# Performance work log

Measured on AMD Instinct MI355X. Metric: run time of the kernel, lower is better.

## Reference

```python
import jax, jax.numpy as jnp
import numpy as np

I, H, O = 64, 256, 24
B, S = 256, 1024


def setup_inputs() -> dict:
    key = jax.random.key(0)
    ks = jax.random.split(key, 9)
    s = lambda *d: 1.0 / np.sqrt(d[0])
    return {
        "x": jax.random.normal(ks[0], (B, S, I), dtype=jnp.float32),
        "Wi": jax.random.normal(ks[1], (I, 4 * H), dtype=jnp.float32) * s(I),
        "Wh": jax.random.normal(ks[2], (H, 4 * H), dtype=jnp.float32) * s(H),
        "b": jnp.zeros((4 * H,), dtype=jnp.float32),
        "attn_W": jax.random.normal(ks[3], (H, H), dtype=jnp.float32) * s(H),
        "attn_b": jnp.zeros((H,), dtype=jnp.float32),
        "v": jax.random.uniform(ks[4], (H,), dtype=jnp.float32) * 0.01,
        "fc_W": jax.random.normal(ks[5], (H, O), dtype=jnp.float32) * s(H),
        "fc_b": jnp.zeros((O,), dtype=jnp.float32),
    }


def _lstm(x, Wi, Wh, b):
    # x: [B, S, I] -> outputs [B, S, H]
    xW = jnp.einsum("bsi,ij->bsj", x, Wi)  # precompute input projections
    Bsz = x.shape[0]
    h0 = jnp.zeros((Bsz, H), x.dtype)
    c0 = jnp.zeros((Bsz, H), x.dtype)

    def step(carry, xt):
        c, h = carry
        z = xt + h @ Wh + b  # [B, 4H]
        i, f, g, o = jnp.split(z, 4, axis=-1)
        c = jax.nn.sigmoid(f) * c + jax.nn.sigmoid(i) * jnp.tanh(g)
        h = jax.nn.sigmoid(o) * jnp.tanh(c)
        return (c, h), h

    _, hs = jax.lax.scan(step, (c0, h0), jnp.swapaxes(xW, 0, 1))
    return jnp.swapaxes(hs, 0, 1)  # [B, S, H]


def reference(x, Wi, Wh, b, attn_W, attn_b, v, fc_W, fc_b):
    lstm_out = _lstm(x, Wi, Wh, b)  # [B, S, H]
    energy = jnp.tanh(lstm_out @ attn_W + attn_b)  # [B, S, H]
    scores = jnp.einsum("bsh,h->bs", energy, v)
    attn = jax.nn.softmax(scores, axis=1)  # [B, S]
    context = jnp.einsum("bs,bsh->bh", attn, lstm_out)
    return context @ fc_W + fc_b  # [B, O]
```

## Files before the change

### kernel.cpp

```cpp
#include <hip/hip_runtime.h>

#define BB 256
#define SS 1024
#define II 64
#define HH 256
#define OO 24
#define NG 16
#define NP 16
#define BT 16

typedef __attribute__((ext_vector_type(8))) short short8;
typedef __attribute__((ext_vector_type(4))) float f32x4;
typedef unsigned long long ull;

#define H_CAP  8192
#define SP_CAP 16384

#define A_HI 0
#define A_LO 8192
#define Z_OF 16384
#define E_OF 20480
#define SMEM_BYTES 98304

#define MFMA(a,b,c) __builtin_amdgcn_mfma_f32_16x16x32_bf16(a,b,c,0,0,0)

__device__ __forceinline__ float fsig(float x)  { return 1.f/(1.f+__expf(-x)); }
__device__ __forceinline__ float ftanh(float x) { return 1.f - 2.f/(__expf(2.f*x)+1.f); }

__device__ __forceinline__ unsigned rne_bf16(float x){
    unsigned u = __float_as_uint(x);
    return (u + 0x7FFFu + ((u>>16)&1u)) >> 16;
}
__device__ __forceinline__ void split_bf(float x, unsigned &hi, unsigned &lo){
    hi = rne_bf16(x);
    lo = rne_bf16(x - __uint_as_float(hi<<16));
}

union U4 { unsigned u[4]; short8 s; };

__device__ __forceinline__ void pack8(const float* v, short8 &H, short8 &L){
    U4 h_, l_;
    #pragma unroll
    for (int i = 0; i < 4; ++i) {
        unsigned a,b,c,d;
        split_bf(v[2*i], a, b); split_bf(v[2*i+1], c, d);
        h_.u[i] = a | (c<<16);
        l_.u[i] = b | (d<<16);
    }
    H = h_.s; L = l_.s;
}

__device__ __forceinline__ ull cld(const ull* p){
    return __hip_atomic_load(p, __ATOMIC_RELAXED, __HIP_MEMORY_SCOPE_AGENT);
}
__device__ __forceinline__ void cst(ull* p, ull v){
    __hip_atomic_store(p, v, __ATOMIC_RELAXED, __HIP_MEMORY_SCOPE_AGENT);
}

__global__ __launch_bounds__(256, 1)
void lstm_fused_kernel(const float* __restrict__ x,  const float* __restrict__ Wi,
                       const float* __restrict__ Wh, const float* __restrict__ bias,
                       const float* __restrict__ aW, const float* __restrict__ ab,
                       const float* __restrict__ av,
                       ull* __restrict__ hx, ull* __restrict__ spx,
                       float* __restrict__ ctxg)
{
    __shared__ __align__(16) char smem[SMEM_BYTES];
    __shared__ int sdead;

    const int tid = threadIdx.x;
    const int w = tid >> 6;
    const int l = tid & 63;
    const int p = blockIdx.x >> 4;
    const int g = blockIdx.x & 15;
    const int b0 = g * BT;

    if (tid == 0) sdead = 0;
    __syncthreads();

    const int n = l & 15;
    const int gcol = w*256 + p*16 + n;
    const int gb = (l>>4)*4 + w;
    const int gd = n;

    short8 BwhH[8], BwhL[8];
    #pragma unroll
    for (int ks = 0; ks < 8; ++ks) {
        U4 H, L;
        #pragma unroll
        for (int i2 = 0; i2 < 4; ++i2) {
            int k0 = ks*32 + (l>>4)*8 + i2*2;
            unsigned h0,l0,h1,l1;
            split_bf(Wh[(size_t)k0*1024 + gcol], h0, l0);
            split_bf(Wh[(size_t)(k0+1)*1024 + gcol], h1, l1);
            H.u[i2] = h0 | (h1<<16);
            L.u[i2] = l0 | (l1<<16);
        }
        BwhH[ks] = H.s; BwhL[ks] = L.s;
    }
    short8 BwiH[2], BwiL[2];
    #pragma unroll
    for (int ks = 0; ks < 2; ++ks) {
        U4 H, L;
        #pragma unroll
        for (int i2 = 0; i2 < 4; ++i2) {
            int k0 = ks*32 + (l>>4)*8 + i2*2;
            unsigned h0,l0,h1,l1;
            split_bf(Wi[(size_t)k0*1024 + gcol], h0, l0);
            split_bf(Wi[(size_t)(k0+1)*1024 + gcol], h1, l1);
            H.u[i2] = h0 | (h1<<16);
            L.u[i2] = l0 | (l1<<16);
        }
        BwiH[ks] = H.s; BwiL[ks] = L.s;
    }
    short8 BwaH[2], BwaL[2];
    #pragma unroll
    for (int j = 0; j < 2; ++j) {
        int ks = 2*w + j;
        U4 H, L;
        #pragma unroll
        for (int i2 = 0; i2 < 4; ++i2) {
            int k0 = ks*32 + (l>>4)*8 + i2*2;
            unsigned h0,l0,h1,l1;
            split_bf(aW[(size_t)k0*256 + p*16 + n], h0, l0);
            split_bf(aW[(size_t)(k0+1)*256 + p*16 + n], h1, l1);
            H.u[i2] = h0 | (h1<<16);
            L.u[i2] = l0 | (l1<<16);
        }
        BwaH[j] = H.s; BwaL[j] = L.s;
    }
    const float bb  = bias[gcol];
    const float vj  = av[p*16 + gd];
    const float abj = ab[p*16 + gd];

    const int po    = tid >> 3;
    const int pbase = (tid & 7) * 2;
    const int wa0 = (po>>2)*1024 + ((po&3)*16 + pbase)*16;
    const int wa1 = wa0 + 16;

    const int D = p*16 + gd;
    const int tau   = (gb>>1) | ((D>>3)<<3);
    const int j_pub = ((gb&1)<<3) | (D&7);

    const int xb = l & 15;
    const int xoct = l >> 4;

    float c_state = 0.f, h1v = 0.f, h2v = 0.f;
    float m_run = -1.0e30f, l_run = 0.f, ctx = 0.f;

    float* zl = (float*)(smem + Z_OF);
    float* el = (float*)(smem + E_OF);

    for (int t = 0; t < SS; ++t) {
        const int par = t & 1;
        const float* xrow = x + ((size_t)(b0 + xb) * SS + t) * II + xoct*8;
        float xv0[8], xv1[8];
        *(float4*)&xv0[0] = *(const float4*)(xrow);
        *(float4*)&xv0[4] = *(const float4*)(xrow + 4);
        *(float4*)&xv1[0] = *(const float4*)(xrow + 32);
        *(float4*)&xv1[4] = *(const float4*)(xrow + 36);

        ull hv[16]; ull spr = 0;
        const ull* hr = hx + ((size_t)(((t-1)&1)*NG + g) * 16) * 256 + tid;
        if (t > 0) {
            #pragma unroll
            for (int j = 0; j < 16; ++j) hv[j] = cld(hr + j*256);
        }
        ull* spp = spx + (size_t)par*4096 + g*256 + gb*16 + gd;
        if (t > 1) spr = cld(spp);

        short8 XH0, XL0, XH1, XL1;
        pack8(xv0, XH0, XL0);
        pack8(xv1, XH1, XL1);
        f32x4 zacc = {bb,bb,bb,bb};
        zacc = MFMA(XH0, BwiH[0], zacc);
        zacc = MFMA(XH0, BwiL[0], zacc);
        zacc = MFMA(XL0, BwiH[0], zacc);
        zacc = MFMA(XH1, BwiH[1], zacc);
        zacc = MFMA(XH1, BwiL[1], zacc);
        zacc = MFMA(XL1, BwiH[1], zacc);

        if (t > 0) {
            const unsigned texp = (unsigned)t;
            unsigned need = 0xFFFFu;
            int rounds = 0;
            while (true) {
                unsigned nn = 0;
                #pragma unroll
                for (int e = 0; e < 16; ++e)
                    if (need & (1u<<e))
                        if ((unsigned)(hv[e]>>32) != texp) nn |= (1u<<e);
                need = nn;
                if (!need || sdead) break;
                if (++rounds > H_CAP) { sdead = 1; break; }
                #pragma unroll
                for (int e = 0; e < 16; ++e)
                    if (need & (1u<<e)) hv[e] = cld(hr + e*256);
            }
            float va[16];
            #pragma unroll
            for (int e = 0; e < 16; ++e) va[e] = __uint_as_float((unsigned)hv[e]);
            short8 H0,L0,H1,L1;
            pack8(&va[0], H0, L0);
            pack8(&va[8], H1, L1);
            *(short8*)(smem + A_HI + wa0) = H0;
            *(short8*)(smem + A_LO + wa0) = L0;
            *(short8*)(smem + A_HI + wa1) = H1;
            *(short8*)(smem + A_LO + wa1) = L1;
        }
        __syncthreads();

        f32x4 zacc1 = {0.f,0.f,0.f,0.f};
        f32x4 eacc  = {0.f,0.f,0.f,0.f};
        if (t > 0) {
            #pragma unroll
            for (int ks = 0; ks < 8; ++ks) {
                short8 ah = *(const short8*)(smem + A_HI + ks*1024 + l*16);
                short8 al = *(const short8*)(smem + A_LO + ks*1024 + l*16);
                if ((ks & 1) == 0) {
                    zacc = MFMA(ah, BwhH[ks], zacc);
                    zacc = MFMA(ah, BwhL[ks], zacc);
                    zacc = MFMA(al, BwhH[ks], zacc);
                } else {
                    zacc1 = MFMA(ah, BwhH[ks], zacc1);
                    zacc1 = MFMA(ah, BwhL[ks], zacc1);
                    zacc1 = MFMA(al, BwhH[ks], zacc1);
                }
                if ((ks>>1) == w) {
                    int jj = ks & 1;
                    eacc = MFMA(ah, BwaH[jj], eacc);
                    eacc = MFMA(ah, BwaL[jj], eacc);
                    eacc = MFMA(al, BwaH[jj], eacc);
                }
            }
        }
        #pragma unroll
        for (int r = 0; r < 4; ++r) zl[w*256 + r*64 + l] = zacc[r] + zacc1[r];
        if (t > 0) {
            #pragma unroll
            for (int r = 0; r < 4; ++r) el[w*256 + r*64 + l] = eacc[r];
        }
        __syncthreads();

        float z0 = zl[0*256 + w*64 + l];
        float z1 = zl[1*256 + w*64 + l];
        float z2 = zl[2*256 + w*64 + l];
        float z3 = zl[3*256 + w*64 + l];
        float ig = fsig(z0), fg = fsig(z1), gv = ftanh(z2), og = fsig(z3);
        c_state = fg*c_state + ig*gv;
        float h = og * ftanh(c_state);

        cst(hx + ((size_t)(par*NG + g) * 16 + j_pub) * 256 + tau,
            ((ull)(unsigned)(t+1) << 32) | (ull)__float_as_uint(h));

        if (t > 0) {
            float e = el[0*256+w*64+l] + el[1*256+w*64+l]
                    + el[2*256+w*64+l] + el[3*256+w*64+l] + abj;
            float scp = vj * ftanh(e);
            scp += __shfl_xor(scp,1); scp += __shfl_xor(scp,2);
            scp += __shfl_xor(scp,4); scp += __shfl_xor(scp,8);
            if (gd == 0)
                cst(spx + (size_t)((t-1)&1)*4096 + g*256 + gb*16 + p,
                    ((ull)(unsigned)t << 32) | (ull)__float_as_uint(scp));
        }
        if (t > 1) {
            const unsigned texp = (unsigned)(t-1);
            int it = 0;
            while ((unsigned)(spr>>32) != texp) {
                if (sdead || ++it > SP_CAP) { sdead = 1; break; }
                spr = cld(spp);
            }
            float s = __uint_as_float((unsigned)spr);
            s += __shfl_xor(s,1); s += __shfl_xor(s,2);
            s += __shfl_xor(s,4); s += __shfl_xor(s,8);
            float m_new = fmaxf(m_run, s);
            float sc = __expf(m_run - m_new);
            float wt = __expf(s - m_new);
            l_run = l_run*sc + wt;
            ctx   = ctx*sc + wt*h2v;
            m_run = m_new;
        }
        h2v = h1v; h1v = h;
    }

    {
        const ull* hr = hx + ((size_t)(((SS-1)&1)*NG + g) * 16) * 256 + tid;
        ull hv[16];
        #pragma unroll
        for (int j = 0; j < 16; ++j) hv[j] = cld(hr + j*256);
        const unsigned texp = (unsigned)SS;
        unsigned need = 0xFFFFu;
        int rounds = 0;
        while (true) {
            unsigned nn = 0;
            #pragma unroll
            for (int e = 0; e < 16; ++e)
                if (need & (1u<<e))
                    if ((unsigned)(hv[e]>>32) != texp) nn |= (1u<<e);
            need = nn;
            if (!need || sdead) break;
            if (++rounds > H_CAP) { sdead = 1; break; }
            #pragma unroll
            for (int e = 0; e < 16; ++e)
                if (need & (1u<<e)) hv[e] = cld(hr + e*256);
        }
        float va[16];
        #pragma unroll
        for (int e = 0; e < 16; ++e) va[e] = __uint_as_float((unsigned)hv[e]);
        short8 H0,L0,H1,L1;
        pack8(&va[0], H0, L0);
        pack8(&va[8], H1, L1);
        *(short8*)(smem + A_HI + wa0) = H0;
        *(short8*)(smem + A_LO + wa0) = L0;
        *(short8*)(smem + A_HI + wa1) = H1;
        *(short8*)(smem + A_LO + wa1) = L1;
        __syncthreads();

        f32x4 eacc = {0.f,0.f,0.f,0.f};
        #pragma unroll
        for (int ks = 0; ks < 8; ++ks) {
            if ((ks>>1) == w) {
                short8 ah = *(const short8*)(smem + A_HI + ks*1024 + l*16);
                short8 al = *(const short8*)(smem + A_LO + ks*1024 + l*16);
                int jj = ks & 1;
                eacc = MFMA(ah, BwaH[jj], eacc);
                eacc = MFMA(ah, BwaL[jj], eacc);
                eacc = MFMA(al, BwaH[jj], eacc);
            }
        }
        #pragma unroll
        for (int r = 0; r < 4; ++r) el[w*256 + r*64 + l] = eacc[r];
        __syncthreads();

        {
            ull* spp2 = spx + (size_t)(SS&1)*4096 + g*256 + gb*16 + gd;
            ull spr = cld(spp2);
            const unsigned te2 = (unsigned)(SS-1);
            int it = 0;
            while ((unsigned)(spr>>32) != te2) {
                if (sdead || ++it > SP_CAP) { sdead = 1; break; }
                spr = cld(spp2);
            }
            float s = __uint_as_float((unsigned)spr);
            s += __shfl_xor(s,1); s += __shfl_xor(s,2);
            s += __shfl_xor(s,4); s += __shfl_xor(s,8);
            float m_new = fmaxf(m_run, s);
            float sc = __expf(m_run - m_new);
            float wt = __expf(s - m_new);
            l_run = l_run*sc + wt;
            ctx   = ctx*sc + wt*h2v;
            m_run = m_new;
        }
        h2v = h1v;
        float e = el[0*256+w*64+l] + el[1*256+w*64+l]
                + el[2*256+w*64+l] + el[3*256+w*64+l] + abj;
        float scp = vj * ftanh(e);
        scp += __shfl_xor(scp,1); scp += __shfl_xor(scp,2);
        scp += __shfl_xor(scp,4); scp += __shfl_xor(scp,8);
        if (gd == 0)
            cst(spx + (size_t)((SS-1)&1)*4096 + g*256 + gb*16 + p,
                ((ull)(unsigned)SS << 32) | (ull)__float_as_uint(scp));
    }

    {
        ull* spp2 = spx + (size_t)((SS-1)&1)*4096 + g*256 + gb*16 + gd;
        ull spr = cld(spp2);
        const unsigned texp = (unsigned)SS;
        int it = 0;
        while ((unsigned)(spr>>32) != texp) {
            if (sdead || ++it > SP_CAP) { sdead = 1; break; }
            spr = cld(spp2);
        }
        float s = __uint_as_float((unsigned)spr);
        s += __shfl_xor(s,1); s += __shfl_xor(s,2);
        s += __shfl_xor(s,4); s += __shfl_xor(s,8);
        float m_new = fmaxf(m_run, s);
        float sc = __expf(m_run - m_new);
        float wt = __expf(s - m_new);
        l_run = l_run*sc + wt;
        ctx   = ctx*sc + wt*h2v;

        ctxg[(size_t)(b0+gb)*HH + p*16 + gd] = ctx / l_run;
    }
}

__global__ __launch_bounds__(64)
void finalize_kernel(const float* __restrict__ ctxg, const float* __restrict__ fcW,
                     const float* __restrict__ fcb, float* __restrict__ out)
{
    __shared__ float cs[HH];
    const int b = blockIdx.x, tid = threadIdx.x;
    *(float4*)&cs[tid*4] = *(const float4*)&ctxg[(size_t)b*HH + tid*4];
    __syncthreads();
    if (tid < OO) {
        float a = fcb[tid];
        #pragma unroll 8
        for (int d = 0; d < HH; ++d) a = fmaf(cs[d], fcW[d*OO + tid], a);
        out[b*OO + tid] = a;
    }
}

extern "C" void kernel_launch(void* const* d_in, const int* in_sizes, int n_in,
                              void* d_out, int out_size, void* d_ws, size_t ws_size,
                              hipStream_t stream)
{
    const float* x      = (const float*)d_in[0];
    const float* Wi     = (const float*)d_in[1];
    const float* Wh     = (const float*)d_in[2];
    const float* bias   = (const float*)d_in[3];
    const float* attn_W = (const float*)d_in[4];
    const float* attn_b = (const float*)d_in[5];
    const float* v      = (const float*)d_in[6];
    const float* fc_W   = (const float*)d_in[7];
    const float* fc_b   = (const float*)d_in[8];
    float* out = (float*)d_out;

    ull*   hx   = (ull*)d_ws;
    ull*   spx  = hx + 2*NG*16*256;
    float* ctxg = (float*)(spx + 8192);

    hipMemsetAsync(hx, 0, (2*NG*16*256 + 8192) * sizeof(ull), stream);

    lstm_fused_kernel<<<dim3(NG*NP), dim3(256), 0, stream>>>(
        x, Wi, Wh, bias, attn_W, attn_b, v, hx, spx, ctxg);
    finalize_kernel<<<dim3(BB), dim3(64), 0, stream>>>(ctxg, fc_W, fc_b, out);
}
```

Measured before the change: 3.523 ms.

## Permute gate columns so gate exchange uses shuffles and pre-split published h

New measurement: 3.569 ms. Within noise of the previous version (+1.3%).

```diff
diff --git a/kernel.cpp b/kernel.cpp
--- a/kernel.cpp
+++ b/kernel.cpp
@@ -18,8 +18,8 @@
 
 #define A_HI 0
 #define A_LO 8192
-#define Z_OF 16384
-#define E_OF 20480
+#define E_OF 16384
+#define HLOC 20480
 #define SMEM_BYTES 98304
 
 #define MFMA(a,b,c) __builtin_amdgcn_mfma_f32_16x16x32_bf16(a,b,c,0,0,0)
@@ -79,9 +79,18 @@
     __syncthreads();
 
     const int n = l & 15;
-    const int gcol = w*256 + p*16 + n;
-    const int gb = (l>>4)*4 + w;
-    const int gd = n;
+    const int gcol = (n>>2)*256 + p*16 + w*4 + (n&3);
+
+    const int sb  = (l>>4)*4 + w;
+    const int sjd = n;
+
+    const int cch = l >> 3, t3 = l & 7;
+    const int b_g  = (t3<<1) | (cch>>2);
+    const int D_gl = 4*w + (cch&3);
+    const int breg = ((t3&1)<<1) | (cch>>2);
+    const int srcb = ((t3>>1)<<4) | (cch&3);
+    const int j_pub = ((b_g&1)<<3) | (D_gl&7);
+    const int tau   = ((2*p + (D_gl>>3))<<3) | t3;
 
     short8 BwhH[8], BwhL[8];
     #pragma unroll
@@ -130,26 +139,22 @@
         BwaH[j] = H.s; BwaL[j] = L.s;
     }
     const float bb  = bias[gcol];
-    const float vj  = av[p*16 + gd];
-    const float abj = ab[p*16 + gd];
+    const float vj  = av[p*16 + sjd];
+    const float abj = ab[p*16 + sjd];
 
     const int po    = tid >> 3;
     const int pbase = (tid & 7) * 2;
     const int wa0 = (po>>2)*1024 + ((po&3)*16 + pbase)*16;
     const int wa1 = wa0 + 16;
 
-    const int D = p*16 + gd;
-    const int tau   = (gb>>1) | ((D>>3)<<3);
-    const int j_pub = ((gb&1)<<3) | (D&7);
-
     const int xb = l & 15;
     const int xoct = l >> 4;
 
-    float c_state = 0.f, h1v = 0.f, h2v = 0.f;
+    float c_state = 0.f;
     float m_run = -1.0e30f, l_run = 0.f, ctx = 0.f;
 
-    float* zl = (float*)(smem + Z_OF);
-    float* el = (float*)(smem + E_OF);
+    float* el   = (float*)(smem + E_OF);
+    float* hloc = (float*)(smem + HLOC);
 
     for (int t = 0; t < SS; ++t) {
         const int par = t & 1;
@@ -166,7 +171,7 @@
             #pragma unroll
             for (int j = 0; j < 16; ++j) hv[j] = cld(hr + j*256);
         }
-        ull* spp = spx + (size_t)par*4096 + g*256 + gb*16 + gd;
+        ull* spp = spx + (size_t)par*4096 + g*256 + sb*16 + sjd;
         if (t > 1) spr = cld(spp);
 
         short8 XH0, XL0, XH1, XL1;
@@ -197,16 +202,20 @@
                 for (int e = 0; e < 16; ++e)
                     if (need & (1u<<e)) hv[e] = cld(hr + e*256);
             }
-            float va[16];
-            #pragma unroll
-            for (int e = 0; e < 16; ++e) va[e] = __uint_as_float((unsigned)hv[e]);
-            short8 H0,L0,H1,L1;
-            pack8(&va[0], H0, L0);
-            pack8(&va[8], H1, L1);
-            *(short8*)(smem + A_HI + wa0) = H0;
-            *(short8*)(smem + A_LO + wa0) = L0;
-            *(short8*)(smem + A_HI + wa1) = H1;
-            *(short8*)(smem + A_LO + wa1) = L1;
+            U4 H0u, L0u, H1u, L1u;
+            #pragma unroll
+            for (int i = 0; i < 4; ++i) {
+                unsigned a = (unsigned)hv[2*i],   b_ = (unsigned)hv[2*i+1];
+                unsigned c = (unsigned)hv[8+2*i], d_ = (unsigned)hv[9+2*i];
+                H0u.u[i] = (a>>16) | (b_ & 0xFFFF0000u);
+                L0u.u[i] = (a & 0xFFFFu) | (b_<<16);
+                H1u.u[i] = (c>>16) | (d_ & 0xFFFF0000u);
+                L1u.u[i] = (c & 0xFFFFu) | (d_<<16);
+            }
+            *(short8*)(smem + A_HI + wa0) = H0u.s;
+            *(short8*)(smem + A_LO + wa0) = L0u.s;
+            *(short8*)(smem + A_HI + wa1) = H1u.s;
+            *(short8*)(smem + A_LO + wa1) = L1u.s;
         }
         __syncthreads();
 
@@ -234,24 +243,41 @@
                 }
             }
         }
-        #pragma unroll
-        for (int r = 0; r < 4; ++r) zl[w*256 + r*64 + l] = zacc[r] + zacc1[r];
-        if (t > 0) {
-            #pragma unroll
-            for (int r = 0; r < 4; ++r) el[w*256 + r*64 + l] = eacc[r];
-        }
-        __syncthreads();
-
-        float z0 = zl[0*256 + w*64 + l];
-        float z1 = zl[1*256 + w*64 + l];
-        float z2 = zl[2*256 + w*64 + l];
-        float z3 = zl[3*256 + w*64 + l];
-        float ig = fsig(z0), fg = fsig(z1), gv = ftanh(z2), og = fsig(z3);
+
+        float zs0 = zacc[0]+zacc1[0], zs1 = zacc[1]+zacc1[1];
+        float zs2 = zacc[2]+zacc1[2], zs3 = zacc[3]+zacc1[3];
+        float zg0,zg1,zg2,zg3;
+        #pragma unroll
+        for (int q = 0; q < 4; ++q) {
+            int srcl = srcb | (q<<2);
+            float v0 = __shfl(zs0, srcl);
+            float v1 = __shfl(zs1, srcl);
+            float v2 = __shfl(zs2, srcl);
+            float v3 = __shfl(zs3, srcl);
+            float vv = (breg==0)? v0 : (breg==1)? v1 : (breg==2)? v2 : v3;
+            if      (q==0) zg0 = vv;
+            else if (q==1) zg1 = vv;
+            else if (q==2) zg2 = vv;
+            else           zg3 = vv;
+        }
+        float ig = fsig(zg0), fg = fsig(zg1), gv = ftanh(zg2), og = fsig(zg3);
         c_state = fg*c_state + ig*gv;
         float h = og * ftanh(c_state);
 
-        cst(hx + ((size_t)(par*NG + g) * 16 + j_pub) * 256 + tau,
-            ((ull)(unsigned)(t+1) << 32) | (ull)__float_as_uint(h));
+        hloc[((t%3)*16 + b_g)*17 + D_gl] = h;
+
+        {
+            unsigned hhi, hlo;
+            split_bf(h, hhi, hlo);
+            cst(hx + ((size_t)(par*NG + g) * 16 + j_pub) * 256 + tau,
+                ((ull)(unsigned)(t+1) << 32) | (ull)((hhi<<16)|hlo));
+        }
+
+        if (t > 0) {
+            #pragma unroll
+            for (int r = 0; r < 4; ++r) el[w*256 + r*64 + l] = eacc[r];
+        }
+        __syncthreads();
 
         if (t > 0) {
             float e = el[0*256+w*64+l] + el[1*256+w*64+l]
@@ -259,8 +285,8 @@
             float scp = vj * ftanh(e);
             scp += __shfl_xor(scp,1); scp += __shfl_xor(scp,2);
             scp += __shfl_xor(scp,4); scp += __shfl_xor(scp,8);
-            if (gd == 0)
-                cst(spx + (size_t)((t-1)&1)*4096 + g*256 + gb*16 + p,
+            if (sjd == 0)
+                cst(spx + (size_t)((t-1)&1)*4096 + g*256 + sb*16 + p,
                     ((ull)(unsigned)t << 32) | (ull)__float_as_uint(scp));
         }
         if (t > 1) {
@@ -273,14 +299,14 @@
             float s = __uint_as_float((unsigned)spr);
             s += __shfl_xor(s,1); s += __shfl_xor(s,2);
             s += __shfl_xor(s,4); s += __shfl_xor(s,8);
+            float hh = hloc[(((t-2)%3)*16 + sb)*17 + sjd];
             float m_new = fmaxf(m_run, s);
             float sc = __expf(m_run - m_new);
             float wt = __expf(s - m_new);
             l_run = l_run*sc + wt;
-            ctx   = ctx*sc + wt*h2v;
+            ctx   = ctx*sc + wt*hh;
             m_run = m_new;
         }
-        h2v = h1v; h1v = h;
     }
 
     {
@@ -304,16 +330,20 @@
             for (int e = 0; e < 16; ++e)
                 if (need & (1u<<e)) hv[e] = cld(hr + e*256);
         }
-        float va[16];
-        #pragma unroll
-        for (int e = 0; e < 16; ++e) va[e] = __uint_as_float((unsigned)hv[e]);
-        short8 H0,L0,H1,L1;
-        pack8(&va[0], H0, L0);
-        pack8(&va[8], H1, L1);
-        *(short8*)(smem + A_HI + wa0) = H0;
-        *(short8*)(smem + A_LO + wa0) = L0;
-        *(short8*)(smem + A_HI + wa1) = H1;
-        *(short8*)(smem + A_LO + wa1) = L1;
+        U4 H0u, L0u, H1u, L1u;
+        #pragma unroll
+        for (int i = 0; i < 4; ++i) {
+            unsigned a = (unsigned)hv[2*i],   b_ = (unsigned)hv[2*i+1];
+            unsigned c = (unsigned)hv[8+2*i], d_ = (unsigned)hv[9+2*i];
+            H0u.u[i] = (a>>16) | (b_ & 0xFFFF0000u);
+            L0u.u[i] = (a & 0xFFFFu) | (b_<<16);
+            H1u.u[i] = (c>>16) | (d_ & 0xFFFF0000u);
+            L1u.u[i] = (c & 0xFFFFu) | (d_<<16);
+        }
+        *(short8*)(smem + A_HI + wa0) = H0u.s;
+        *(short8*)(smem + A_LO + wa0) = L0u.s;
+        *(short8*)(smem + A_HI + wa1) = H1u.s;
+        *(short8*)(smem + A_LO + wa1) = L1u.s;
         __syncthreads();
 
         f32x4 eacc = {0.f,0.f,0.f,0.f};
@@ -333,7 +363,7 @@
         __syncthreads();
 
         {
-            ull* spp2 = spx + (size_t)(SS&1)*4096 + g*256 + gb*16 + gd;
+            ull* spp2 = spx + (size_t)(SS&1)*4096 + g*256 + sb*16 + sjd;
             ull spr = cld(spp2);
             const unsigned te2 = (unsigned)(SS-1);
             int it = 0;
@@ -344,26 +374,26 @@
             float s = __uint_as_float((unsigned)spr);
             s += __shfl_xor(s,1); s += __shfl_xor(s,2);
             s += __shfl_xor(s,4); s += __shfl_xor(s,8);
+            float hh = hloc[(((SS-2)%3)*16 + sb)*17 + sjd];
             float m_new = fmaxf(m_run, s);
             float sc = __expf(m_run - m_new);
             float wt = __expf(s - m_new);
             l_run = l_run*sc + wt;
-            ctx   = ctx*sc + wt*h2v;
+            ctx   = ctx*sc + wt*hh;
             m_run = m_new;
         }
-        h2v = h1v;
         float e = el[0*256+w*64+l] + el[1*256+w*64+l]
                 + el[2*256+w*64+l] + el[3*256+w*64+l] + abj;
         float scp = vj * ftanh(e);
         scp += __shfl_xor(scp,1); scp += __shfl_xor(scp,2);
         scp += __shfl_xor(scp,4); scp += __shfl_xor(scp,8);
-        if (gd == 0)
-            cst(spx + (size_t)((SS-1)&1)*4096 + g*256 + gb*16 + p,
+        if (sjd == 0)
+            cst(spx + (size_t)((SS-1)&1)*4096 + g*256 + sb*16 + p,
                 ((ull)(unsigned)SS << 32) | (ull)__float_as_uint(scp));
     }
 
     {
-        ull* spp2 = spx + (size_t)((SS-1)&1)*4096 + g*256 + gb*16 + gd;
+        ull* spp2 = spx + (size_t)((SS-1)&1)*4096 + g*256 + sb*16 + sjd;
         ull spr = cld(spp2);
         const unsigned texp = (unsigned)SS;
         int it = 0;
@@ -374,13 +404,14 @@
         float s = __uint_as_float((unsigned)spr);
         s += __shfl_xor(s,1); s += __shfl_xor(s,2);
         s += __shfl_xor(s,4); s += __shfl_xor(s,8);
+        float hh = hloc[(((SS-1)%3)*16 + sb)*17 + sjd];
         float m_new = fmaxf(m_run, s);
         float sc = __expf(m_run - m_new);
         float wt = __expf(s - m_new);
         l_run = l_run*sc + wt;
-        ctx   = ctx*sc + wt*h2v;
-
-        ctxg[(size_t)(b0+gb)*HH + p*16 + gd] = ctx / l_run;
+        ctx   = ctx*sc + wt*hh;
+
+        ctxg[(size_t)(b0+sb)*HH + p*16 + sjd] = ctx / l_run;
     }
 }
 
```

## Interleave two independent batch streams per block to hide cross-block latency

Applied to the files above, without the earlier changes.

Result: slower. 6.389 ms (+81.4%).

```diff
diff --git a/kernel.cpp b/kernel.cpp
--- a/kernel.cpp
+++ b/kernel.cpp
@@ -5,9 +5,9 @@
 #define II 64
 #define HH 256
 #define OO 24
-#define NG 16
+#define NG 32
 #define NP 16
-#define BT 16
+#define BT 8
 
 typedef __attribute__((ext_vector_type(8))) short short8;
 typedef __attribute__((ext_vector_type(4))) float f32x4;
@@ -16,10 +16,14 @@
 #define H_CAP  8192
 #define SP_CAP 16384
 
-#define A_HI 0
-#define A_LO 8192
-#define Z_OF 16384
-#define E_OF 20480
+#define AHI_A 0
+#define ALO_A 8192
+#define AHI_B 16384
+#define ALO_B 24576
+#define ZL_A  32768
+#define EL_A  36864
+#define ZL_B  40960
+#define EL_B  45056
 #define SMEM_BYTES 98304
 
 #define MFMA(a,b,c) __builtin_amdgcn_mfma_f32_16x16x32_bf16(a,b,c,0,0,0)
@@ -57,217 +61,122 @@
     __hip_atomic_store(p, v, __ATOMIC_RELAXED, __HIP_MEMORY_SCOPE_AGENT);
 }
 
-__global__ __launch_bounds__(256, 1)
-void lstm_fused_kernel(const float* __restrict__ x,  const float* __restrict__ Wi,
-                       const float* __restrict__ Wh, const float* __restrict__ bias,
-                       const float* __restrict__ aW, const float* __restrict__ ab,
-                       const float* __restrict__ av,
-                       ull* __restrict__ hx, ull* __restrict__ spx,
-                       float* __restrict__ ctxg)
-{
-    __shared__ __align__(16) char smem[SMEM_BYTES];
-    __shared__ int sdead;
-
-    const int tid = threadIdx.x;
-    const int w = tid >> 6;
-    const int l = tid & 63;
-    const int p = blockIdx.x >> 4;
-    const int g = blockIdx.x & 15;
-    const int b0 = g * BT;
-
-    if (tid == 0) sdead = 0;
-    __syncthreads();
-
-    const int n = l & 15;
-    const int gcol = w*256 + p*16 + n;
-    const int gb = (l>>4)*4 + w;
-    const int gd = n;
-
-    short8 BwhH[8], BwhL[8];
-    #pragma unroll
-    for (int ks = 0; ks < 8; ++ks) {
+template<int AHI, int ALO, int ZLo, int ELo>
+__device__ __forceinline__ void stream_step(
+    int t, int tid, int w, int l, int p, int g, int b0,
+    const float* __restrict__ x, char* smem, int* sdp,
+    const short8* BwhH, const short8* BwhL,
+    const short8* BwiH, const short8* BwiL,
+    const short8* BwaH, const short8* BwaL,
+    float bbv, float vj, float abj,
+    ull* hx, ull* spx, ull* hv,
+    float& c_state, float& h1v, float& h2v,
+    float& m_run, float& l_run, float& ctx)
+{
+    const int xb = l & 7, xoct = l >> 4;
+    const float* xrow = x + ((size_t)(b0 + xb) * SS + t) * II + xoct*8;
+    float xv0[8], xv1[8];
+    *(float4*)&xv0[0] = *(const float4*)(xrow);
+    *(float4*)&xv0[4] = *(const float4*)(xrow + 4);
+    *(float4*)&xv1[0] = *(const float4*)(xrow + 32);
+    *(float4*)&xv1[4] = *(const float4*)(xrow + 36);
+
+    const int sb  = tid >> 4;
+    const int sjd = tid & 15;
+    ull spr = 0;
+    ull* spp = spx + (size_t)((t&1)*NG + g)*128 + (sb&7)*16 + sjd;
+    if (t > 1 && tid < 128) spr = cld(spp);
+
+    short8 XH0,XL0,XH1,XL1;
+    pack8(xv0,XH0,XL0); pack8(xv1,XH1,XL1);
+    f32x4 zacc = {bbv,bbv,bbv,bbv};
+    zacc = MFMA(XH0,BwiH[0],zacc); zacc = MFMA(XH0,BwiL[0],zacc); zacc = MFMA(XL0,BwiH[0],zacc);
+    zacc = MFMA(XH1,BwiH[1],zacc); zacc = MFMA(XH1,BwiL[1],zacc); zacc = MFMA(XL1,BwiH[1],zacc);
+
+    if (t > 0) {
+        const ull* hr = hx + ((size_t)(((t-1)&1)*NG + g)*8)*256 + tid;
+        const unsigned texp = (unsigned)t;
+        unsigned need = 0xFFu; int rounds = 0;
+        while (true) {
+            unsigned nn = 0;
+            #pragma unroll
+            for (int e = 0; e < 8; ++e)
+                if (need & (1u<<e))
+                    if ((unsigned)(hv[e]>>32) != texp) nn |= (1u<<e);
+            need = nn;
+            if (!need || *sdp) break;
+            if (++rounds > H_CAP) { *sdp = 1; break; }
+            #pragma unroll
+            for (int e = 0; e < 8; ++e)
+                if (need & (1u<<e)) hv[e] = cld(hr + e*256);
+        }
         U4 H, L;
         #pragma unroll
-        for (int i2 = 0; i2 < 4; ++i2) {
-            int k0 = ks*32 + (l>>4)*8 + i2*2;
-            unsigned h0,l0,h1,l1;
-            split_bf(Wh[(size_t)k0*1024 + gcol], h0, l0);
-            split_bf(Wh[(size_t)(k0+1)*1024 + gcol], h1, l1);
-            H.u[i2] = h0 | (h1<<16);
-            L.u[i2] = l0 | (l1<<16);
-        }
-        BwhH[ks] = H.s; BwhL[ks] = L.s;
-    }
-    short8 BwiH[2], BwiL[2];
-    #pragma unroll
-    for (int ks = 0; ks < 2; ++ks) {
-        U4 H, L;
-        #pragma unroll
-        for (int i2 = 0; i2 < 4; ++i2) {
-            int k0 = ks*32 + (l>>4)*8 + i2*2;
-            unsigned h0,l0,h1,l1;
-            split_bf(Wi[(size_t)k0*1024 + gcol], h0, l0);
-            split_bf(Wi[(size_t)(k0+1)*1024 + gcol], h1, l1);
-            H.u[i2] = h0 | (h1<<16);
-            L.u[i2] = l0 | (l1<<16);
-        }
-        BwiH[ks] = H.s; BwiL[ks] = L.s;
-    }
-    short8 BwaH[2], BwaL[2];
-    #pragma unroll
-    for (int j = 0; j < 2; ++j) {
-        int ks = 2*w + j;
-        U4 H, L;
-        #pragma unroll
-        for (int i2 = 0; i2 < 4; ++i2) {
-            int k0 = ks*32 + (l>>4)*8 + i2*2;
-            unsigned h0,l0,h1,l1;
-            split_bf(aW[(size_t)k0*256 + p*16 + n], h0, l0);
-            split_bf(aW[(size_t)(k0+1)*256 + p*16 + n], h1, l1);
-            H.u[i2] = h0 | (h1<<16);
-            L.u[i2] = l0 | (l1<<16);
-        }
-        BwaH[j] = H.s; BwaL[j] = L.s;
-    }
-    const float bb  = bias[gcol];
-    const float vj  = av[p*16 + gd];
-    const float abj = ab[p*16 + gd];
-
-    const int po    = tid >> 3;
-    const int pbase = (tid & 7) * 2;
-    const int wa0 = (po>>2)*1024 + ((po&3)*16 + pbase)*16;
-    const int wa1 = wa0 + 16;
-
-    const int D = p*16 + gd;
-    const int tau   = (gb>>1) | ((D>>3)<<3);
-    const int j_pub = ((gb&1)<<3) | (D&7);
-
-    const int xb = l & 15;
-    const int xoct = l >> 4;
-
-    float c_state = 0.f, h1v = 0.f, h2v = 0.f;
-    float m_run = -1.0e30f, l_run = 0.f, ctx = 0.f;
-
-    float* zl = (float*)(smem + Z_OF);
-    float* el = (float*)(smem + E_OF);
-
-    for (int t = 0; t < SS; ++t) {
-        const int par = t & 1;
-        const float* xrow = x + ((size_t)(b0 + xb) * SS + t) * II + xoct*8;
-        float xv0[8], xv1[8];
-        *(float4*)&xv0[0] = *(const float4*)(xrow);
-        *(float4*)&xv0[4] = *(const float4*)(xrow + 4);
-        *(float4*)&xv1[0] = *(const float4*)(xrow + 32);
-        *(float4*)&xv1[4] = *(const float4*)(xrow + 36);
-
-        ull hv[16]; ull spr = 0;
-        const ull* hr = hx + ((size_t)(((t-1)&1)*NG + g) * 16) * 256 + tid;
-        if (t > 0) {
-            #pragma unroll
-            for (int j = 0; j < 16; ++j) hv[j] = cld(hr + j*256);
-        }
-        ull* spp = spx + (size_t)par*4096 + g*256 + gb*16 + gd;
-        if (t > 1) spr = cld(spp);
-
-        short8 XH0, XL0, XH1, XL1;
-        pack8(xv0, XH0, XL0);
-        pack8(xv1, XH1, XL1);
-        f32x4 zacc = {bb,bb,bb,bb};
-        zacc = MFMA(XH0, BwiH[0], zacc);
-        zacc = MFMA(XH0, BwiL[0], zacc);
-        zacc = MFMA(XL0, BwiH[0], zacc);
-        zacc = MFMA(XH1, BwiH[1], zacc);
-        zacc = MFMA(XH1, BwiL[1], zacc);
-        zacc = MFMA(XL1, BwiH[1], zacc);
-
-        if (t > 0) {
-            const unsigned texp = (unsigned)t;
-            unsigned need = 0xFFFFu;
-            int rounds = 0;
-            while (true) {
-                unsigned nn = 0;
-                #pragma unroll
-                for (int e = 0; e < 16; ++e)
-                    if (need & (1u<<e))
-                        if ((unsigned)(hv[e]>>32) != texp) nn |= (1u<<e);
-                need = nn;
-                if (!need || sdead) break;
-                if (++rounds > H_CAP) { sdead = 1; break; }
-                #pragma unroll
-                for (int e = 0; e < 16; ++e)
-                    if (need & (1u<<e)) hv[e] = cld(hr + e*256);
+        for (int i = 0; i < 4; ++i) {
+            unsigned a = (unsigned)hv[2*i], b_ = (unsigned)hv[2*i+1];
+            H.u[i] = (a>>16) | (b_ & 0xFFFF0000u);
+            L.u[i] = (a & 0xFFFFu) | (b_<<16);
+        }
+        const int po_c = tid & 31, bb_c = tid >> 5;
+        const int wa = ((po_c>>2)*64 + (po_c&3)*16 + bb_c)*16;
+        *(short8*)(smem + AHI + wa) = H.s;
+        *(short8*)(smem + ALO + wa) = L.s;
+    }
+    __syncthreads();
+
+    f32x4 zacc1 = {0.f,0.f,0.f,0.f}, eacc = {0.f,0.f,0.f,0.f};
+    if (t > 0) {
+        #pragma unroll
+        for (int ks = 0; ks < 8; ++ks) {
+            short8 ah = *(const short8*)(smem + AHI + ks*1024 + l*16);
+            short8 al = *(const short8*)(smem + ALO + ks*1024 + l*16);
+            if ((ks & 1) == 0) {
+                zacc  = MFMA(ah,BwhH[ks],zacc);  zacc  = MFMA(ah,BwhL[ks],zacc);  zacc  = MFMA(al,BwhH[ks],zacc);
+            } else {
+                zacc1 = MFMA(ah,BwhH[ks],zacc1); zacc1 = MFMA(ah,BwhL[ks],zacc1); zacc1 = MFMA(al,BwhH[ks],zacc1);
             }
-            float va[16];
-            #pragma unroll
-            for (int e = 0; e < 16; ++e) va[e] = __uint_as_float((unsigned)hv[e]);
-            short8 H0,L0,H1,L1;
-            pack8(&va[0], H0, L0);
-            pack8(&va[8], H1, L1);
-            *(short8*)(smem + A_HI + wa0) = H0;
-            *(short8*)(smem + A_LO + wa0) = L0;
-            *(short8*)(smem + A_HI + wa1) = H1;
-            *(short8*)(smem + A_LO + wa1) = L1;
-        }
-        __syncthreads();
-
-        f32x4 zacc1 = {0.f,0.f,0.f,0.f};
-        f32x4 eacc  = {0.f,0.f,0.f,0.f};
-        if (t > 0) {
-            #pragma unroll
-            for (int ks = 0; ks < 8; ++ks) {
-                short8 ah = *(const short8*)(smem + A_HI + ks*1024 + l*16);
-                short8 al = *(const short8*)(smem + A_LO + ks*1024 + l*16);
-                if ((ks & 1) == 0) {
-                    zacc = MFMA(ah, BwhH[ks], zacc);
-                    zacc = MFMA(ah, BwhL[ks], zacc);
-                    zacc = MFMA(al, BwhH[ks], zacc);
-                } else {
-                    zacc1 = MFMA(ah, BwhH[ks], zacc1);
-                    zacc1 = MFMA(ah, BwhL[ks], zacc1);
-                    zacc1 = MFMA(al, BwhH[ks], zacc1);
-                }
-                if ((ks>>1) == w) {
-                    int jj = ks & 1;
-                    eacc = MFMA(ah, BwaH[jj], eacc);
-                    eacc = MFMA(ah, BwaL[jj], eacc);
-                    eacc = MFMA(al, BwaH[jj], eacc);
-                }
+            if ((ks>>1) == w) {
+                int jj = ks & 1;
+                eacc = MFMA(ah,BwaH[jj],eacc); eacc = MFMA(ah,BwaL[jj],eacc); eacc = MFMA(al,BwaH[jj],eacc);
             }
         }
-        #pragma unroll
-        for (int r = 0; r < 4; ++r) zl[w*256 + r*64 + l] = zacc[r] + zacc1[r];
-        if (t > 0) {
-            #pragma unroll
-            for (int r = 0; r < 4; ++r) el[w*256 + r*64 + l] = eacc[r];
-        }
-        __syncthreads();
-
-        float z0 = zl[0*256 + w*64 + l];
-        float z1 = zl[1*256 + w*64 + l];
-        float z2 = zl[2*256 + w*64 + l];
-        float z3 = zl[3*256 + w*64 + l];
+    }
+    float* zl = (float*)(smem + ZLo);
+    float* el = (float*)(smem + ELo);
+    #pragma unroll
+    for (int r = 0; r < 4; ++r) zl[w*256 + r*64 + l] = zacc[r] + zacc1[r];
+    if (t > 0) {
+        #pragma unroll
+        for (int r = 0; r < 4; ++r) el[w*256 + r*64 + l] = eacc[r];
+    }
+    __syncthreads();
+
+    if (tid < 128) {
+        const int zi = (sb&3)*64 + (sb>>2)*16 + sjd;
+        float z0 = zl[0*256+zi], z1 = zl[1*256+zi], z2 = zl[2*256+zi], z3 = zl[3*256+zi];
         float ig = fsig(z0), fg = fsig(z1), gv = ftanh(z2), og = fsig(z3);
         c_state = fg*c_state + ig*gv;
         float h = og * ftanh(c_state);
 
-        cst(hx + ((size_t)(par*NG + g) * 16 + j_pub) * 256 + tau,
-            ((ull)(unsigned)(t+1) << 32) | (ull)__float_as_uint(h));
+        unsigned hhi, hlo; split_bf(h, hhi, hlo);
+        const int D = p*16 + sjd;
+        cst(hx + ((size_t)((t&1)*NG + g)*8 + (D&7))*256 + (sb*32 + (D>>3)),
+            ((ull)(unsigned)(t+1) << 32) | (ull)((hhi<<16)|hlo));
 
         if (t > 0) {
-            float e = el[0*256+w*64+l] + el[1*256+w*64+l]
-                    + el[2*256+w*64+l] + el[3*256+w*64+l] + abj;
+            float e = el[0*256+zi] + el[1*256+zi] + el[2*256+zi] + el[3*256+zi] + abj;
             float scp = vj * ftanh(e);
             scp += __shfl_xor(scp,1); scp += __shfl_xor(scp,2);
             scp += __shfl_xor(scp,4); scp += __shfl_xor(scp,8);
-            if (gd == 0)
-                cst(spx + (size_t)((t-1)&1)*4096 + g*256 + gb*16 + p,
+            if (sjd == 0)
+                cst(spx + (size_t)(((t-1)&1)*NG + g)*128 + sb*16 + p,
                     ((ull)(unsigned)t << 32) | (ull)__float_as_uint(scp));
         }
         if (t > 1) {
-            const unsigned texp = (unsigned)(t-1);
+            const unsigned texp2 = (unsigned)(t-1);
             int it = 0;
-            while ((unsigned)(spr>>32) != texp) {
-                if (sdead || ++it > SP_CAP) { sdead = 1; break; }
+            while ((unsigned)(spr>>32) != texp2) {
+                if (*sdp || ++it > SP_CAP) { *sdp = 1; break; }
                 spr = cld(spp);
             }
             float s = __uint_as_float((unsigned)spr);
@@ -282,64 +191,69 @@
         }
         h2v = h1v; h1v = h;
     }
-
-    {
-        const ull* hr = hx + ((size_t)(((SS-1)&1)*NG + g) * 16) * 256 + tid;
-        ull hv[16];
-        #pragma unroll
-        for (int j = 0; j < 16; ++j) hv[j] = cld(hr + j*256);
-        const unsigned texp = (unsigned)SS;
-        unsigned need = 0xFFFFu;
-        int rounds = 0;
-        while (true) {
-            unsigned nn = 0;
-            #pragma unroll
-            for (int e = 0; e < 16; ++e)
-                if (need & (1u<<e))
-                    if ((unsigned)(hv[e]>>32) != texp) nn |= (1u<<e);
-            need = nn;
-            if (!need || sdead) break;
-            if (++rounds > H_CAP) { sdead = 1; break; }
-            #pragma unroll
-            for (int e = 0; e < 16; ++e)
-                if (need & (1u<<e)) hv[e] = cld(hr + e*256);
-        }
-        float va[16];
-        #pragma unroll
-        for (int e = 0; e < 16; ++e) va[e] = __uint_as_float((unsigned)hv[e]);
-        short8 H0,L0,H1,L1;
-        pack8(&va[0], H0, L0);
-        pack8(&va[8], H1, L1);
-        *(short8*)(smem + A_HI + wa0) = H0;
-        *(short8*)(smem + A_LO + wa0) = L0;
-        *(short8*)(smem + A_HI + wa1) = H1;
-        *(short8*)(smem + A_LO + wa1) = L1;
-        __syncthreads();
-
-        f32x4 eacc = {0.f,0.f,0.f,0.f};
-        #pragma unroll
-        for (int ks = 0; ks < 8; ++ks) {
-            if ((ks>>1) == w) {
-                short8 ah = *(const short8*)(smem + A_HI + ks*1024 + l*16);
-                short8 al = *(const short8*)(smem + A_LO + ks*1024 + l*16);
-                int jj = ks & 1;
-                eacc = MFMA(ah, BwaH[jj], eacc);
-                eacc = MFMA(ah, BwaL[jj], eacc);
-                eacc = MFMA(al, BwaH[jj], eacc);
-            }
-        }
-        #pragma unroll
-        for (int r = 0; r < 4; ++r) el[w*256 + r*64 + l] = eacc[r];
-        __syncthreads();
-
+}
+
+template<int AHI, int ALO, int ELo>
+__device__ __forceinline__ void stream_epiA(
+    int tid, int w, int l, int p, int g, char* smem, int* sdp,
+    const short8* BwaH, const short8* BwaL,
+    float vj, float abj, ull* hx, ull* spx, ull* hv,
+    float& h1v, float& h2v, float& m_run, float& l_run, float& ctx)
+{
+    const ull* hr = hx + ((size_t)(((SS-1)&1)*NG + g)*8)*256 + tid;
+    const unsigned texp = (unsigned)SS;
+    unsigned need = 0xFFu; int rounds = 0;
+    while (true) {
+        unsigned nn = 0;
+        #pragma unroll
+        for (int e = 0; e < 8; ++e)
+            if (need & (1u<<e))
+                if ((unsigned)(hv[e]>>32) != texp) nn |= (1u<<e);
+        need = nn;
+        if (!need || *sdp) break;
+        if (++rounds > H_CAP) { *sdp = 1; break; }
+        #pragma unroll
+        for (int e = 0; e < 8; ++e)
+            if (need & (1u<<e)) hv[e] = cld(hr + e*256);
+    }
+    U4 H, L;
+    #pragma unroll
+    for (int i = 0; i < 4; ++i) {
+        unsigned a = (unsigned)hv[2*i], b_ = (unsigned)hv[2*i+1];
+        H.u[i] = (a>>16) | (b_ & 0xFFFF0000u);
+        L.u[i] = (a & 0xFFFFu) | (b_<<16);
+    }
+    const int po_c = tid & 31, bb_c = tid >> 5;
+    const int wa = ((po_c>>2)*64 + (po_c&3)*16 + bb_c)*16;
+    *(short8*)(smem + AHI + wa) = H.s;
+    *(short8*)(smem + ALO + wa) = L.s;
+    __syncthreads();
+
+    f32x4 eacc = {0.f,0.f,0.f,0.f};
+    #pragma unroll
+    for (int ks = 0; ks < 8; ++ks)
+        if ((ks>>1) == w) {
+            short8 ah = *(const short8*)(smem + AHI + ks*1024 + l*16);
+            short8 al = *(const short8*)(smem + ALO + ks*1024 + l*16);
+            int jj = ks & 1;
+            eacc = MFMA(ah,BwaH[jj],eacc); eacc = MFMA(ah,BwaL[jj],eacc); eacc = MFMA(al,BwaH[jj],eacc);
+        }
+    float* el = (float*)(smem + ELo);
+    #pragma unroll
+    for (int r = 0; r < 4; ++r) el[w*256 + r*64 + l] = eacc[r];
+    __syncthreads();
+
+    if (tid < 128) {
+        const int sb = tid >> 4, sjd = tid & 15;
+        const int zi = (sb&3)*64 + (sb>>2)*16 + sjd;
         {
-            ull* spp2 = spx + (size_t)(SS&1)*4096 + g*256 + gb*16 + gd;
-            ull spr = cld(spp2);
+            ull* spp = spx + (size_t)((SS&1)*NG + g)*128 + sb*16 + sjd;
+            ull spr = cld(spp);
             const unsigned te2 = (unsigned)(SS-1);
             int it = 0;
             while ((unsigned)(spr>>32) != te2) {
-                if (sdead || ++it > SP_CAP) { sdead = 1; break; }
-                spr = cld(spp2);
+                if (*sdp || ++it > SP_CAP) { *sdp = 1; break; }
+                spr = cld(spp);
             }
             float s = __uint_as_float((unsigned)spr);
             s += __shfl_xor(s,1); s += __shfl_xor(s,2);
@@ -352,24 +266,29 @@
             m_run = m_new;
         }
         h2v = h1v;
-        float e = el[0*256+w*64+l] + el[1*256+w*64+l]
-                + el[2*256+w*64+l] + el[3*256+w*64+l] + abj;
+        float e = el[0*256+zi] + el[1*256+zi] + el[2*256+zi] + el[3*256+zi] + abj;
         float scp = vj * ftanh(e);
         scp += __shfl_xor(scp,1); scp += __shfl_xor(scp,2);
         scp += __shfl_xor(scp,4); scp += __shfl_xor(scp,8);
-        if (gd == 0)
-            cst(spx + (size_t)((SS-1)&1)*4096 + g*256 + gb*16 + p,
+        if (sjd == 0)
+            cst(spx + (size_t)(((SS-1)&1)*NG + g)*128 + sb*16 + p,
                 ((ull)(unsigned)SS << 32) | (ull)__float_as_uint(scp));
     }
-
-    {
-        ull* spp2 = spx + (size_t)((SS-1)&1)*4096 + g*256 + gb*16 + gd;
-        ull spr = cld(spp2);
+}
+
+__device__ __forceinline__ void stream_epiB(
+    int tid, int p, int g, ull* spx, int* sdp,
+    float h2v, float m_run, float l_run, float ctx, float* ctxg)
+{
+    if (tid < 128) {
+        const int sb = tid >> 4, sjd = tid & 15;
+        ull* spp = spx + (size_t)(((SS-1)&1)*NG + g)*128 + sb*16 + sjd;
+        ull spr = cld(spp);
         const unsigned texp = (unsigned)SS;
         int it = 0;
         while ((unsigned)(spr>>32) != texp) {
-            if (sdead || ++it > SP_CAP) { sdead = 1; break; }
-            spr = cld(spp2);
+            if (*sdp || ++it > SP_CAP) { *sdp = 1; break; }
+            spr = cld(spp);
         }
         float s = __uint_as_float((unsigned)spr);
         s += __shfl_xor(s,1); s += __shfl_xor(s,2);
@@ -379,9 +298,120 @@
         float wt = __expf(s - m_new);
         l_run = l_run*sc + wt;
         ctx   = ctx*sc + wt*h2v;
-
-        ctxg[(size_t)(b0+gb)*HH + p*16 + gd] = ctx / l_run;
-    }
+        ctxg[(size_t)(g*BT + sb)*HH + p*16 + sjd] = ctx / l_run;
+    }
+}
+
+__global__ __launch_bounds__(256, 1)
+void lstm_fused_kernel(const float* __restrict__ x,  const float* __restrict__ Wi,
+                       const float* __restrict__ Wh, const float* __restrict__ bias,
+                       const float* __restrict__ aW, const float* __restrict__ ab,
+                       const float* __restrict__ av,
+                       ull* __restrict__ hx, ull* __restrict__ spx,
+                       float* __restrict__ ctxg)
+{
+    __shared__ __align__(16) char smem[SMEM_BYTES];
+    __shared__ int sdead;
+
+    const int tid = threadIdx.x;
+    const int w = tid >> 6;
+    const int l = tid & 63;
+    const int p = blockIdx.x & 15;
+    const int gA = (blockIdx.x >> 4) * 2;
+    const int gB = gA + 1;
+    const int b0A = gA * BT, b0B = gB * BT;
+
+    if (tid == 0) sdead = 0;
+    __syncthreads();
+
+    const int n = l & 15;
+    const int gcol = w*256 + p*16 + n;
+
+    short8 BwhH[8], BwhL[8];
+    #pragma unroll
+    for (int ks = 0; ks < 8; ++ks) {
+        U4 H, L;
+        #pragma unroll
+        for (int i2 = 0; i2 < 4; ++i2) {
+            int k0 = ks*32 + (l>>4)*8 + i2*2;
+            unsigned h0,l0,h1,l1;
+            split_bf(Wh[(size_t)k0*1024 + gcol], h0, l0);
+            split_bf(Wh[(size_t)(k0+1)*1024 + gcol], h1, l1);
+            H.u[i2] = h0 | (h1<<16);
+            L.u[i2] = l0 | (l1<<16);
+        }
+        BwhH[ks] = H.s; BwhL[ks] = L.s;
+    }
+    short8 BwiH[2], BwiL[2];
+    #pragma unroll
+    for (int ks = 0; ks < 2; ++ks) {
+        U4 H, L;
+        #pragma unroll
+        for (int i2 = 0; i2 < 4; ++i2) {
+            int k0 = ks*32 + (l>>4)*8 + i2*2;
+            unsigned h0,l0,h1,l1;
+            split_bf(Wi[(size_t)k0*1024 + gcol], h0, l0);
+            split_bf(Wi[(size_t)(k0+1)*1024 + gcol], h1, l1);
+            H.u[i2] = h0 | (h1<<16);
+            L.u[i2] = l0 | (l1<<16);
+        }
+        BwiH[ks] = H.s; BwiL[ks] = L.s;
+    }
+    short8 BwaH[2], BwaL[2];
+    #pragma unroll
+    for (int j = 0; j < 2; ++j) {
+        int ks = 2*w + j;
+        U4 H, L;
+        #pragma unroll
+        for (int i2 = 0; i2 < 4; ++i2) {
+            int k0 = ks*32 + (l>>4)*8 + i2*2;
+            unsigned h0,l0,h1,l1;
+            split_bf(aW[(size_t)k0*256 + p*16 + n], h0, l0);
+            split_bf(aW[(size_t)(k0+1)*256 + p*16 + n], h1, l1);
+            H.u[i2] = h0 | (h1<<16);
+            L.u[i2] = l0 | (l1<<16);
+        }
+        BwaH[j] = H.s; BwaL[j] = L.s;
+    }
+    const float bbv = bias[gcol];
+    const float vj  = av[p*16 + (tid & 15)];
+    const float abj = ab[p*16 + (tid & 15)];
+
+    float cA=0.f, h1A=0.f, h2A=0.f, mA=-1.0e30f, lA=0.f, cxA=0.f;
+    float cB=0.f, h1B=0.f, h2B=0.f, mB=-1.0e30f, lB=0.f, cxB=0.f;
+    ull hvA[8], hvB[8];
+
+    for (int t = 0; t < SS; ++t) {
+        if (t > 0) {
+            const ull* hrB = hx + ((size_t)(((t-1)&1)*NG + gB)*8)*256 + tid;
+            #pragma unroll
+            for (int j = 0; j < 8; ++j) hvB[j] = cld(hrB + j*256);
+        }
+        stream_step<AHI_A,ALO_A,ZL_A,EL_A>(t, tid, w, l, p, gA, b0A, x, smem, &sdead,
+            BwhH,BwhL,BwiH,BwiL,BwaH,BwaL, bbv,vj,abj, hx,spx, hvA,
+            cA,h1A,h2A,mA,lA,cxA);
+
+        {
+            const ull* hrA = hx + ((size_t)((t&1)*NG + gA)*8)*256 + tid;
+            #pragma unroll
+            for (int j = 0; j < 8; ++j) hvA[j] = cld(hrA + j*256);
+        }
+        stream_step<AHI_B,ALO_B,ZL_B,EL_B>(t, tid, w, l, p, gB, b0B, x, smem, &sdead,
+            BwhH,BwhL,BwiH,BwiL,BwaH,BwaL, bbv,vj,abj, hx,spx, hvB,
+            cB,h1B,h2B,mB,lB,cxB);
+    }
+
+    {
+        const ull* hrB = hx + ((size_t)(((SS-1)&1)*NG + gB)*8)*256 + tid;
+        #pragma unroll
+        for (int j = 0; j < 8; ++j) hvB[j] = cld(hrB + j*256);
+    }
+    stream_epiA<AHI_A,ALO_A,EL_A>(tid,w,l,p,gA, smem,&sdead, BwaH,BwaL, vj,abj,
+                                  hx,spx, hvA, h1A,h2A,mA,lA,cxA);
+    stream_epiA<AHI_B,ALO_B,EL_B>(tid,w,l,p,gB, smem,&sdead, BwaH,BwaL, vj,abj,
+                                  hx,spx, hvB, h1B,h2B,mB,lB,cxB);
+    stream_epiB(tid,p,gA,spx,&sdead, h2A,mA,lA,cxA, ctxg);
+    stream_epiB(tid,p,gB,spx,&sdead, h2B,mB,lB,cxB, ctxg);
 }
 
 __global__ __launch_bounds__(64)
@@ -416,12 +446,12 @@
     float* out = (float*)d_out;
 
     ull*   hx   = (ull*)d_ws;
-    ull*   spx  = hx + 2*NG*16*256;
-    float* ctxg = (float*)(spx + 8192);
-
-    hipMemsetAsync(hx, 0, (2*NG*16*256 + 8192) * sizeof(ull), stream);
-
-    lstm_fused_kernel<<<dim3(NG*NP), dim3(256), 0, stream>>>(
+    ull*   spx  = hx + 2*NG*8*256;
+    float* ctxg = (float*)(spx + 2*NG*128);
+
+    hipMemsetAsync(hx, 0, (2*NG*8*256 + 2*NG*128) * sizeof(ull), stream);
+
+    lstm_fused_kernel<<<dim3(256), dim3(256), 0, stream>>>(
         x, Wi, Wh, bias, attn_W, attn_b, v, hx, spx, ctxg);
     finalize_kernel<<<dim3(BB), dim3(64), 0, stream>>>(ctxg, fc_W, fc_b, out);
 }
```
